# Kernel tuning notes

Measured on AMD Instinct MI355X. Metric: run time of the kernel, lower is better.

## Reference

```python
import jax, jax.numpy as jnp
import numpy as np

EPS = 1e-05

def _self_cost_cosine(embs):
    # embs: [n, d] -> cost: [n, n]
    energy = jnp.sqrt(jnp.sum(embs ** 2, axis=1, keepdims=True))  # [n,1]
    gram = embs @ embs.T
    denom = energy @ energy.T + EPS
    return 1.0 - jnp.exp(-5.0 * (1.0 - gram / denom))

def _mutual_cost_cosine(embs1, embs2):
    e1 = jnp.sqrt(jnp.sum(embs1 ** 2, axis=1, keepdims=True))
    e2 = jnp.sqrt(jnp.sum(embs2 ** 2, axis=1, keepdims=True))
    gram = embs1 @ embs2.T
    denom = e1 @ e2.T + EPS
    return 1.0 - jnp.exp(-(1.0 - gram / denom))

def _tensor_times_mat_l2(cost_s, cost_t, trans, mu_s, mu_t):
    f1 = (cost_s ** 2) @ mu_s            # [n1,1], broadcasts over columns
    f2 = mu_t.T @ (cost_t ** 2).T        # [1,n2], broadcasts over rows
    return f1 + f2 - 2.0 * (cost_s @ trans @ cost_t.T)

def _similarity_l2(cost_pred, cost_truth):
    return jnp.sum((cost_pred - cost_truth) ** 2 * jnp.exp(-cost_truth))

def _orthogonal(embs):
    d = embs.shape[1]
    orth = embs.T @ embs - jnp.eye(d, dtype=embs.dtype)
    return jnp.sum(orth ** 2)

def setup_inputs() -> dict:
    key = jax.random.key(0)
    ks = jax.random.split(key, 9)
    num1, num2, dim, n = 50000, 50000, 128, 4096
    emb1_w = jax.random.uniform(ks[0], (num1, dim), jnp.float32, -1.0 / dim, 1.0 / dim)
    emb2_w = jax.random.uniform(ks[1], (num2, dim), jnp.float32, -1.0 / dim, 1.0 / dim)
    index1 = jax.random.randint(ks[2], (n,), 0, num1, dtype=jnp.int64 if jax.config.jax_enable_x64 else jnp.int32)
    index2 = jax.random.randint(ks[3], (n,), 0, num2, dtype=jnp.int64 if jax.config.jax_enable_x64 else jnp.int32)
    trans = jax.random.uniform(ks[4], (n, n), jnp.float32) / (n * n)
    mu_s = jax.random.uniform(ks[5], (n, 1), jnp.float32) / n
    mu_t = jax.random.uniform(ks[6], (n, 1), jnp.float32) / n
    cost1 = jax.random.uniform(ks[7], (n, n), jnp.float32)
    cost2 = jax.random.uniform(ks[8], (n, n), jnp.float32)
    return {"index1": index1, "index2": index2, "trans": trans, "mu_s": mu_s,
            "mu_t": mu_t, "cost1": cost1, "cost2": cost2,
            "emb1_w": emb1_w, "emb2_w": emb2_w}

def reference(index1, index2, trans, mu_s, mu_t, cost1, cost2, emb1_w, emb2_w):
    embs1 = emb1_w[index1]  # [n1, d]
    embs2 = emb2_w[index2]  # [n2, d]
    cost_s = _self_cost_cosine(embs1)
    cost_t = _self_cost_cosine(embs2)
    cost_st = _mutual_cost_cosine(embs1, embs2)
    cost = _tensor_times_mat_l2(cost_s, cost_t, trans, mu_s, mu_t)
    d_gw = jnp.sum(cost * trans)
    d_w = jnp.sum(cost_st * trans)
    regularizer = (_similarity_l2(cost_s, cost1) + _similarity_l2(cost_t, cost2)
                   + _orthogonal(embs1) + _orthogonal(embs2))
    return (d_gw, d_w, regularizer)
```

## Files before the change

kernel.cpp:

```cpp
#include <hip/hip_runtime.h>
#include <math.h>

#define N 4096
#define D 128
#define FEPS 1e-5f
#define C0F 0.993262053f
#define NT 64

typedef __attribute__((ext_vector_type(8))) short bf16x8;
typedef __attribute__((ext_vector_type(4))) float f32x4;

__device__ __forceinline__ unsigned short f2bf(float f) {
    union { float f; unsigned u; } v; v.f = f;
    unsigned r = v.u + 0x7fffu + ((v.u >> 16) & 1u);
    return (unsigned short)(r >> 16);
}
__device__ __forceinline__ float bf2f(short s) {
    union { unsigned u; float f; } v; v.u = ((unsigned)(unsigned short)s) << 16;
    return v.f;
}

__device__ __forceinline__ void async16(void* lds, const void* g) {
    __builtin_amdgcn_global_load_lds(
        (const __attribute__((address_space(1))) unsigned int*)g,
        (__attribute__((address_space(3))) unsigned int*)lds, 16, 0, 0);
}

__device__ __forceinline__ double block_reduce256(double v, double* red) {
    int t = threadIdx.x;
    red[t] = v;
    __syncthreads();
    #pragma unroll
    for (int s = 128; s > 0; s >>= 1) {
        if (t < s) red[t] += red[t + s];
        __syncthreads();
    }
    double r = red[0];
    __syncthreads();
    return r;
}

__device__ __forceinline__ double block_reduce512(double v, double* red) {
    int t = threadIdx.x;
    red[t] = v;
    __syncthreads();
    #pragma unroll
    for (int s = 256; s > 0; s >>= 1) {
        if (t < s) red[t] += red[t + s];
        __syncthreads();
    }
    double r = red[0];
    __syncthreads();
    return r;
}

__global__ void gather_energy(const float* __restrict__ W, const int* __restrict__ idx,
                              float* __restrict__ E, float* __restrict__ energy) {
    int i = blockIdx.x, t = threadIdx.x;
    float v = W[(size_t)idx[i] * D + t];
    E[(size_t)i * D + t] = v;
    float sq = v * v;
    #pragma unroll
    for (int o = 32; o > 0; o >>= 1) sq += __shfl_down(sq, o);
    __shared__ float s2[2];
    if ((t & 63) == 0) s2[t >> 6] = sq;
    __syncthreads();
    if (t == 0) energy[i] = sqrtf(s2[0] + s2[1]);
}

__global__ void trans_convert(const float* __restrict__ T,
                              unsigned short* __restrict__ Ta,
                              unsigned short* __restrict__ Tb,
                              float* __restrict__ trow, float* __restrict__ tcol,
                              double* __restrict__ sc) {
    __shared__ float cs[4][256];
    __shared__ float ws[4];
    int t = threadIdx.x;
    int cb = blockIdx.x * 64 + (t & 63);
    int rb = blockIdx.y * 4 + (t >> 6);
    int r0 = rb * 4, c0 = cb * 4;
    float vv[4][4];
    #pragma unroll
    for (int i = 0; i < 4; ++i) {
        float4 r4 = *(const float4*)&T[(size_t)(r0 + i) * N + c0];
        vv[i][0] = r4.x; vv[i][1] = r4.y; vv[i][2] = r4.z; vv[i][3] = r4.w;
    }
    #pragma unroll
    for (int i = 0; i < 4; ++i) {
        int r = r0 + i;
        size_t slot = ((size_t)(r >> 4) * (N / 8) + (c0 >> 3)) * 128 + (r & 15) * 8 + (c0 & 7);
        short4 s;
        s.x = (short)f2bf(vv[i][0]); s.y = (short)f2bf(vv[i][1]);
        s.z = (short)f2bf(vv[i][2]); s.w = (short)f2bf(vv[i][3]);
        *(short4*)&Ta[slot] = s;
    }
    #pragma unroll
    for (int j = 0; j < 4; ++j) {
        int n = c0 + j;
        size_t slot = ((size_t)(n >> 4) * (N / 8) + (r0 >> 3)) * 128 + (n & 15) * 8 + (r0 & 7);
        short4 s;
        s.x = (short)f2bf(vv[0][j]); s.y = (short)f2bf(vv[1][j]);
        s.z = (short)f2bf(vv[2][j]); s.w = (short)f2bf(vv[3][j]);
        *(short4*)&Tb[slot] = s;
    }
    float wtot = 0.f;
    #pragma unroll
    for (int i = 0; i < 4; ++i) {
        float s = vv[i][0] + vv[i][1] + vv[i][2] + vv[i][3];
        #pragma unroll
        for (int o = 32; o > 0; o >>= 1) s += __shfl_down(s, o);
        if ((t & 63) == 0) { atomicAdd(&trow[r0 + i], s); wtot += s; }
    }
    if ((t & 63) == 0) ws[t >> 6] = wtot;
    int g = t >> 6;
    #pragma unroll
    for (int j = 0; j < 4; ++j)
        cs[g][(t & 63) * 4 + j] = vv[0][j] + vv[1][j] + vv[2][j] + vv[3][j];
    __syncthreads();
    float csum = cs[0][t] + cs[1][t] + cs[2][t] + cs[3][t];
    atomicAdd(&tcol[blockIdx.x * 256 + t], csum);
    if (t == 0) atomicAdd(&sc[5], (double)(ws[0] + ws[1] + ws[2] + ws[3]));
}

template <int SELF>
__global__ __launch_bounds__(256) void cost_kernel(
        const float* __restrict__ EA, const float* __restrict__ EB,
        const float* __restrict__ ea, const float* __restrict__ eb,
        const float* __restrict__ ref_or_trans,
        const float* __restrict__ mu, const float* __restrict__ tsum,
        unsigned short* __restrict__ outD, double* __restrict__ sc) {
    __shared__ float As[16][68];
    __shared__ float Bs[16][68];
    __shared__ double red[256];
    int t = threadIdx.x;
    int tx = t & 15, ty = t >> 4;
    int bi = blockIdx.y * 64, bj = blockIdx.x * 64;
    float acc[4][4] = {};
    for (int kk = 0; kk < D; kk += 16) {
        #pragma unroll
        for (int r = 0; r < 4; ++r) {
            int e = t + 256 * r;
            int ar = e >> 4, ac = e & 15;
            As[ac][ar] = EA[(size_t)(bi + ar) * D + kk + ac];
            Bs[ac][ar] = EB[(size_t)(bj + ar) * D + kk + ac];
        }
        __syncthreads();
        #pragma unroll
        for (int k = 0; k < 16; ++k) {
            float4 av = *(const float4*)&As[k][ty * 4];
            float4 bv = *(const float4*)&Bs[k][tx * 4];
            float a[4] = {av.x, av.y, av.z, av.w};
            float b[4] = {bv.x, bv.y, bv.z, bv.w};
            #pragma unroll
            for (int u = 0; u < 4; ++u)
                #pragma unroll
                for (int v = 0; v < 4; ++v)
                    acc[u][v] = fmaf(a[u], b[v], acc[u][v]);
        }
        __syncthreads();
    }
    float eav[4], ebv[4];
    #pragma unroll
    for (int u = 0; u < 4; ++u) eav[u] = ea[bi + ty * 4 + u];
    #pragma unroll
    for (int v = 0; v < 4; ++v) ebv[v] = eb[bj + tx * 4 + v];

    double l1 = 0.0, l2 = 0.0;
    #pragma unroll
    for (int u = 0; u < 4; ++u) {
        int ri = bi + ty * 4 + u;
        float cv[4];
        #pragma unroll
        for (int v = 0; v < 4; ++v) {
            int ci = bj + tx * 4 + v;
            size_t id = (size_t)ri * N + ci;
            float denom = eav[u] * ebv[v] + FEPS;
            float cosv = acc[u][v] / denom;
            if (SELF) {
                float c = 1.f - expf(-5.f * (1.f - cosv));
                cv[v] = c;
                float rc = ref_or_trans[id];
                float dd = c - rc;
                l1 += (double)(dd * dd * expf(-rc));
                l2 += (double)(c * c) * (double)mu[ci] * (double)tsum[ri];
            } else {
                float c = 1.f - expf(-(1.f - cosv));
                l1 += (double)c * (double)ref_or_trans[id];
            }
        }
        if (SELF) {
            int ci0 = bj + tx * 4;
            size_t slot = ((size_t)(ri >> 4) * (N / 8) + (ci0 >> 3)) * 128 + (ri & 15) * 8 + (ci0 & 7);
            short4 s;
            s.x = (short)f2bf(cv[0] - C0F); s.y = (short)f2bf(cv[1] - C0F);
            s.z = (short)f2bf(cv[2] - C0F); s.w = (short)f2bf(cv[3] - C0F);
            *(short4*)&outD[slot] = s;
        }
    }
    double s1 = block_reduce256(l1, red);
    if (SELF) {
        double s2v = block_reduce256(l2, red);
        if (t == 0) { atomicAdd(&sc[0], s1); atomicAdd(&sc[1], s2v); }
    } else {
        if (t == 0) atomicAdd(&sc[3], s1);
    }
}

#define MFMA16(a, b, c) __builtin_amdgcn_mfma_f32_16x16x32_bf16(a, b, c, 0, 0, 0)

template <int STORE>
__global__ __launch_bounds__(512, 2) void gemm_mfma(
        const unsigned short* __restrict__ Ag, const unsigned short* __restrict__ Bg,
        unsigned short* __restrict__ Pdb,
        const float* __restrict__ trow, const float* __restrict__ tcol,
        double* __restrict__ sc) {
    __shared__ __align__(16) char Lds[131072];
    __shared__ double red[512];
    const int t = threadIdx.x, l = t & 63;
    const int w = __builtin_amdgcn_readfirstlane(t >> 6);
    const int wm = w >> 2, wn = w & 3;
    const int lid = blockIdx.x;
    const int swz = (lid & 7) * 32 + (lid >> 3);
    const int by = swz >> 4, bx = swz & 15;
    const size_t GRP = (size_t)(N / 8) * 256;

    const char* aBase = (const char*)Ag + ((size_t)by * 16 + w) * GRP + (size_t)l * 16;
    const char* bBase = (const char*)Bg + ((size_t)bx * 16 + w) * GRP + (size_t)l * 16;

#define ISSUE_A(KH, TT) do {                                                   \
    char* _d = Lds + ((TT) & 1) * 65536 + (KH) * 16384 + w * 1024;             \
    const char* _g = aBase + (size_t)(TT) * 2048 + (KH) * 1024;                \
    async16(_d, _g); async16(_d + 8192, _g + 8 * GRP); } while (0)
#define ISSUE_B(KH, TT) do {                                                   \
    char* _d = Lds + ((TT) & 1) * 65536 + 32768 + (KH) * 16384 + w * 1024;     \
    const char* _g = bBase + (size_t)(TT) * 2048 + (KH) * 1024;                \
    async16(_d, _g); async16(_d + 8192, _g + 8 * GRP); } while (0)

    f32x4 acc[8][4];
    #pragma unroll
    for (int i = 0; i < 8; ++i)
        #pragma unroll
        for (int j = 0; j < 4; ++j)
            acc[i][j] = (f32x4){0.f, 0.f, 0.f, 0.f};

    ISSUE_A(0, 0); ISSUE_B(0, 0); ISSUE_A(1, 0); ISSUE_B(1, 0); ISSUE_A(0, 1);
    asm volatile("s_waitcnt vmcnt(6)" ::: "memory");
    __builtin_amdgcn_s_barrier();
    asm volatile("" ::: "memory");

    bf16x8 af[8];
    const char* Albase = Lds + wm * 8192;
    const char* Blbase = Lds + 32768 + wn * 4096;

    for (int tt = 0; tt < NT; ++tt) {
        const int bufo = (tt & 1) * 65536;
        {
            const char* Ab = Albase + bufo;
            const char* Bb = Blbase + bufo;
            #pragma unroll
            for (int mf = 0; mf < 8; ++mf)
                af[mf] = *(const bf16x8*)(Ab + mf * 1024 + l * 16);
            bf16x8 b0 = *(const bf16x8*)(Bb + l * 16);
            bf16x8 b1 = *(const bf16x8*)(Bb + 1024 + l * 16);
            if (tt + 1 < NT) ISSUE_B(0, tt + 1);
            __builtin_amdgcn_s_setprio(1);
            #pragma unroll
            for (int mf = 0; mf < 8; ++mf) {
                acc[mf][0] = MFMA16(af[mf], b0, acc[mf][0]);
                acc[mf][1] = MFMA16(af[mf], b1, acc[mf][1]);
            }
            __builtin_amdgcn_s_setprio(0);
            asm volatile("" ::: "memory");
            __builtin_amdgcn_s_barrier();
            asm volatile("" ::: "memory");
        }
        {
            const char* Bb = Blbase + bufo + 2048;
            bf16x8 b0 = *(const bf16x8*)(Bb + l * 16);
            bf16x8 b1 = *(const bf16x8*)(Bb + 1024 + l * 16);
            if (tt + 1 < NT) ISSUE_A(1, tt + 1);
            __builtin_amdgcn_s_setprio(1);
            #pragma unroll
            for (int mf = 0; mf < 8; ++mf) {
                acc[mf][2] = MFMA16(af[mf], b0, acc[mf][2]);
                acc[mf][3] = MFMA16(af[mf], b1, acc[mf][3]);
            }
            __builtin_amdgcn_s_setprio(0);
            if (tt < NT - 1) { asm volatile("s_waitcnt vmcnt(6)" ::: "memory"); }
            else             { asm volatile("s_waitcnt vmcnt(0)" ::: "memory"); }
            asm volatile("" ::: "memory");
            __builtin_amdgcn_s_barrier();
            asm volatile("" ::: "memory");
        }
        {
            const char* Ab = Albase + bufo + 16384;
            const char* Bb = Blbase + bufo + 16384;
            #pragma unroll
            for (int mf = 0; mf < 8; ++mf)
                af[mf] = *(const bf16x8*)(Ab + mf * 1024 + l * 16);
            bf16x8 b0 = *(const bf16x8*)(Bb + l * 16);
            bf16x8 b1 = *(const bf16x8*)(Bb + 1024 + l * 16);
            if (tt + 1 < NT) ISSUE_B(1, tt + 1);
            __builtin_amdgcn_s_setprio(1);
            #pragma unroll
            for (int mf = 0; mf < 8; ++mf) {
                acc[mf][0] = MFMA16(af[mf], b0, acc[mf][0]);
                acc[mf][1] = MFMA16(af[mf], b1, acc[mf][1]);
            }
            __builtin_amdgcn_s_setprio(0);
            asm volatile("" ::: "memory");
            __builtin_amdgcn_s_barrier();
            asm volatile("" ::: "memory");
        }
        {
            const char* Bb = Blbase + bufo + 16384 + 2048;
            bf16x8 b0 = *(const bf16x8*)(Bb + l * 16);
            bf16x8 b1 = *(const bf16x8*)(Bb + 1024 + l * 16);
            if (tt + 2 < NT) ISSUE_A(0, tt + 2);
            __builtin_amdgcn_s_setprio(1);
            #pragma unroll
            for (int mf = 0; mf < 8; ++mf) {
                acc[mf][2] = MFMA16(af[mf], b0, acc[mf][2]);
                acc[mf][3] = MFMA16(af[mf], b1, acc[mf][3]);
            }
            __builtin_amdgcn_s_setprio(0);
            if (tt < NT - 2)       { asm volatile("s_waitcnt vmcnt(6)" ::: "memory"); }
            else if (tt == NT - 2) { asm volatile("s_waitcnt vmcnt(4)" ::: "memory"); }
            asm volatile("" ::: "memory");
            __builtin_amdgcn_s_barrier();
            asm volatile("" ::: "memory");
        }
    }
#undef ISSUE_A
#undef ISSUE_B

    const size_t base = ((size_t)(by * 16 + bx)) * 65536 + (size_t)w * 8192;
    if (STORE) {
        #pragma unroll
        for (int mf = 0; mf < 8; ++mf)
            #pragma unroll
            for (int nf = 0; nf < 4; ++nf) {
                f32x4 a = acc[mf][nf];
                short4 s;
                s.x = (short)f2bf(a[0]); s.y = (short)f2bf(a[1]);
                s.z = (short)f2bf(a[2]); s.w = (short)f2bf(a[3]);
                *(short4*)&Pdb[base + (size_t)(mf * 4 + nf) * 256 + (size_t)l * 4] = s;
            }
    } else {
        double t1 = 0.0, t2 = 0.0, t3 = 0.0;
        const int quad = l >> 4, lan = l & 15;
        #pragma unroll
        for (int mf = 0; mf < 8; ++mf) {
            const int ib = by * 256 + wm * 128 + mf * 16 + quad * 4;
            float4 tr4 = *(const float4*)&trow[ib];
            float trv[4] = {tr4.x, tr4.y, tr4.z, tr4.w};
            #pragma unroll
            for (int nf = 0; nf < 4; ++nf) {
                const int j = bx * 256 + wn * 64 + nf * 16 + lan;
                const float tcj = tcol[j];
                short4 p = *(const short4*)&Pdb[base + (size_t)(mf * 4 + nf) * 256 + (size_t)l * 4];
                float pf[4] = {bf2f(p.x), bf2f(p.y), bf2f(p.z), bf2f(p.w)};
                #pragma unroll
                for (int r = 0; r < 4; ++r) {
                    double x = (double)acc[mf][nf][r];
                    t1 += (double)tcj * x;
                    t2 += (double)trv[r] * (double)pf[r];
                    t3 += x * (double)pf[r];
                }
            }
        }
        double s1 = block_reduce512(t1, red);
        double s2 = block_reduce512(t2, red);
        double s3 = block_reduce512(t3, red);
        if (t == 0) {
            atomicAdd(&sc[6], s1);
            atomicAdd(&sc[7], s2);
            atomicAdd(&sc[2], s3);
        }
    }
}

__global__ __launch_bounds__(256) void gram_partial(const float* __restrict__ E,
                                                    float* __restrict__ G) {
    __shared__ float Es[16][132];
    int t = threadIdx.x, tx = t & 15, ty = t >> 4;
    int i0 = blockIdx.x * 128;
    float acc[8][8] = {};
    for (int kk = 0; kk < 128; kk += 16) {
        #pragma unroll
        for (int r = 0; r < 2; ++r) {
            int q = t + 256 * r;
            int row = q >> 5, c4 = (q & 31) * 4;
            *(float4*)&Es[row][c4] = *(const float4*)&E[(size_t)(i0 + kk + row) * D + c4];
        }
        __syncthreads();
        #pragma unroll
        for (int k = 0; k < 16; ++k) {
            float a[8], b[8];
            *(float4*)&a[0] = *(const float4*)&Es[k][ty * 8];
            *(float4*)&a[4] = *(const float4*)&Es[k][ty * 8 + 4];
            *(float4*)&b[0] = *(const float4*)&Es[k][tx * 8];
            *(float4*)&b[4] = *(const float4*)&Es[k][tx * 8 + 4];
            #pragma unroll
            for (int u = 0; u < 8; ++u)
                #pragma unroll
                for (int v = 0; v < 8; ++v)
                    acc[u][v] = fmaf(a[u], b[v], acc[u][v]);
        }
        __syncthreads();
    }
    #pragma unroll
    for (int u = 0; u < 8; ++u)
        #pragma unroll
        for (int v = 0; v < 8; ++v)
            atomicAdd(&G[(size_t)(ty * 8 + u) * D + tx * 8 + v], acc[u][v]);
}

__global__ void orth_final(const float* __restrict__ G, double* __restrict__ sc) {
    __shared__ double red[256];
    const float* g = G + (size_t)blockIdx.x * D * D;
    int t = threadIdx.x;
    double s = 0.0;
    for (int q = t; q < D * D; q += 256) {
        float v = g[q] - ((q % (D + 1)) == 0 ? 1.f : 0.f);
        s += (double)v * (double)v;
    }
    double r = block_reduce256(s, red);
    if (t == 0) atomicAdd(&sc[4], r);
}

__global__ void finalize(const double* __restrict__ sc, float* __restrict__ out) {
    if (threadIdx.x == 0) {
        const double C0 = (double)C0F;
        double S = sc[5];
        double pq = C0 * C0 * S * S + C0 * sc[6] + C0 * sc[7] + sc[2];
        out[0] = (float)(sc[1] - 2.0 * pq);
        out[1] = (float)sc[3];
        out[2] = (float)(sc[0] + sc[4]);
    }
}

extern "C" void kernel_launch(void* const* d_in, const int* in_sizes, int n_in,
                              void* d_out, int out_size, void* d_ws, size_t ws_size,
                              hipStream_t stream) {
    const int*   index1 = (const int*)d_in[0];
    const int*   index2 = (const int*)d_in[1];
    const float* trans  = (const float*)d_in[2];
    const float* mu_s   = (const float*)d_in[3];
    const float* mu_t   = (const float*)d_in[4];
    const float* cost1  = (const float*)d_in[5];
    const float* cost2  = (const float*)d_in[6];
    const float* emb1_w = (const float*)d_in[7];
    const float* emb2_w = (const float*)d_in[8];
    float* out = (float*)d_out;

    char* w = (char*)d_ws;
    double* sc  = (double*)w;
    float* tcol = (float*)(w + 256);
    float* trow = (float*)(w + 16640);
    float* e1   = (float*)(w + 33024);
    float* e2   = (float*)(w + 49408);
    float* E1   = (float*)(w + 65792);
    float* E2   = (float*)(w + 2162944);
    unsigned short* Ds  = (unsigned short*)(w + 4260096);
    unsigned short* Ta  = (unsigned short*)(w + 37814528);
    unsigned short* Tb  = (unsigned short*)(w + 71368960);
    unsigned short* Pdb = (unsigned short*)(w + 104923392);
    float* Gbuf = (float*)(w + 37814528);

    hipMemsetAsync(d_ws, 0, 33024, stream);

    gather_energy<<<N, D, 0, stream>>>(emb1_w, index1, E1, e1);
    gather_energy<<<N, D, 0, stream>>>(emb2_w, index2, E2, e2);
    trans_convert<<<dim3(16, 256), 256, 0, stream>>>(trans, Ta, Tb, trow, tcol, sc);

    dim3 g64(N / 64, N / 64);

    cost_kernel<1><<<g64, 256, 0, stream>>>(E1, E1, e1, e1, cost1, mu_s, trow, Ds, sc);
    gemm_mfma<1><<<256, 512, 0, stream>>>(Ds, Tb, Pdb, nullptr, nullptr, sc);
    cost_kernel<1><<<g64, 256, 0, stream>>>(E2, E2, e2, e2, cost2, mu_t, tcol, Ds, sc);
    gemm_mfma<0><<<256, 512, 0, stream>>>(Ta, Ds, Pdb, trow, tcol, sc);
    cost_kernel<0><<<g64, 256, 0, stream>>>(E1, E2, e1, e2, trans, nullptr, nullptr, nullptr, sc);
    hipMemsetAsync(Gbuf, 0, 2 * D * D * sizeof(float), stream);
    gram_partial<<<32, 256, 0, stream>>>(E1, Gbuf);
    gram_partial<<<32, 256, 0, stream>>>(E2, Gbuf + D * D);
    orth_final<<<2, 256, 0, stream>>>(Gbuf, sc);

    finalize<<<1, 64, 0, stream>>>(sc, out);
}
```

Before: 954.9 us.

## Restructure MFMA main loop into M-quarter phases with deeper async prefetch

The GEMM inner loop now splits each k-half into two phases over half the M fragments, each using all four B fragments, instead of phases over half the N fragments. Each phase does 16 MFMAs on 4 A plus 4 B registers, which lowers live fragment registers. Global-to-LDS prefetch is moved earlier: B for tile tt+2 is issued one iteration ahead, and the vmcnt thresholds are raised to match. Extra barriers per phase and lgkmcnt waits are added, which adds sync cost and makes correctness depend on the new buffer-reuse ordering.

Result: slower. 982.4 us (+2.9%).

```diff
diff --git a/kernel.cpp b/kernel.cpp
--- a/kernel.cpp
+++ b/kernel.cpp
@@ -223,9 +223,10 @@
     const int swz = (lid & 7) * 32 + (lid >> 3);
     const int by = swz >> 4, bx = swz & 15;
     const size_t GRP = (size_t)(N / 8) * 256;
-
-    const char* aBase = (const char*)Ag + ((size_t)by * 16 + w) * GRP + (size_t)l * 16;
-    const char* bBase = (const char*)Bg + ((size_t)bx * 16 + w) * GRP + (size_t)l * 16;
+    const int l16 = l * 16;
+
+    const char* aBase = (const char*)Ag + ((size_t)by * 16 + w) * GRP + (size_t)l16;
+    const char* bBase = (const char*)Bg + ((size_t)bx * 16 + w) * GRP + (size_t)l16;
 
 #define ISSUE_A(KH, TT) do {                                                   \
     char* _d = Lds + ((TT) & 1) * 65536 + (KH) * 16384 + w * 1024;             \
@@ -243,96 +244,86 @@
         for (int j = 0; j < 4; ++j)
             acc[i][j] = (f32x4){0.f, 0.f, 0.f, 0.f};
 
-    ISSUE_A(0, 0); ISSUE_B(0, 0); ISSUE_A(1, 0); ISSUE_B(1, 0); ISSUE_A(0, 1);
-    asm volatile("s_waitcnt vmcnt(6)" ::: "memory");
+    ISSUE_A(0, 0); ISSUE_B(0, 0); ISSUE_A(1, 0); ISSUE_B(1, 0);
+    ISSUE_A(0, 1); ISSUE_B(0, 1);
+    asm volatile("s_waitcnt vmcnt(8)" ::: "memory");
     __builtin_amdgcn_s_barrier();
     asm volatile("" ::: "memory");
 
-    bf16x8 af[8];
     const char* Albase = Lds + wm * 8192;
     const char* Blbase = Lds + 32768 + wn * 4096;
 
+    bf16x8 aq[4], b0, b1, b2, b3;
+
+#define MFMA_Q(MB) do {                                                        \
+    _Pragma("unroll")                                                          \
+    for (int _i = 0; _i < 4; ++_i) {                                           \
+        acc[(MB) + _i][0] = MFMA16(aq[_i], b0, acc[(MB) + _i][0]);             \
+        acc[(MB) + _i][1] = MFMA16(aq[_i], b1, acc[(MB) + _i][1]);             \
+        acc[(MB) + _i][2] = MFMA16(aq[_i], b2, acc[(MB) + _i][2]);             \
+        acc[(MB) + _i][3] = MFMA16(aq[_i], b3, acc[(MB) + _i][3]);             \
+    } } while (0)
+
+#define REGION_END                                                             \
+    asm volatile("s_waitcnt lgkmcnt(0)" ::: "memory");                         \
+    __builtin_amdgcn_s_barrier();                                              \
+    asm volatile("" ::: "memory");
+
     for (int tt = 0; tt < NT; ++tt) {
         const int bufo = (tt & 1) * 65536;
-        {
-            const char* Ab = Albase + bufo;
-            const char* Bb = Blbase + bufo;
-            #pragma unroll
-            for (int mf = 0; mf < 8; ++mf)
-                af[mf] = *(const bf16x8*)(Ab + mf * 1024 + l * 16);
-            bf16x8 b0 = *(const bf16x8*)(Bb + l * 16);
-            bf16x8 b1 = *(const bf16x8*)(Bb + 1024 + l * 16);
-            if (tt + 1 < NT) ISSUE_B(0, tt + 1);
-            __builtin_amdgcn_s_setprio(1);
-            #pragma unroll
-            for (int mf = 0; mf < 8; ++mf) {
-                acc[mf][0] = MFMA16(af[mf], b0, acc[mf][0]);
-                acc[mf][1] = MFMA16(af[mf], b1, acc[mf][1]);
-            }
-            __builtin_amdgcn_s_setprio(0);
-            asm volatile("" ::: "memory");
-            __builtin_amdgcn_s_barrier();
-            asm volatile("" ::: "memory");
-        }
-        {
-            const char* Bb = Blbase + bufo + 2048;
-            bf16x8 b0 = *(const bf16x8*)(Bb + l * 16);
-            bf16x8 b1 = *(const bf16x8*)(Bb + 1024 + l * 16);
-            if (tt + 1 < NT) ISSUE_A(1, tt + 1);
-            __builtin_amdgcn_s_setprio(1);
-            #pragma unroll
-            for (int mf = 0; mf < 8; ++mf) {
-                acc[mf][2] = MFMA16(af[mf], b0, acc[mf][2]);
-                acc[mf][3] = MFMA16(af[mf], b1, acc[mf][3]);
-            }
-            __builtin_amdgcn_s_setprio(0);
-            if (tt < NT - 1) { asm volatile("s_waitcnt vmcnt(6)" ::: "memory"); }
-            else             { asm volatile("s_waitcnt vmcnt(0)" ::: "memory"); }
-            asm volatile("" ::: "memory");
-            __builtin_amdgcn_s_barrier();
-            asm volatile("" ::: "memory");
-        }
-        {
-            const char* Ab = Albase + bufo + 16384;
-            const char* Bb = Blbase + bufo + 16384;
-            #pragma unroll
-            for (int mf = 0; mf < 8; ++mf)
-                af[mf] = *(const bf16x8*)(Ab + mf * 1024 + l * 16);
-            bf16x8 b0 = *(const bf16x8*)(Bb + l * 16);
-            bf16x8 b1 = *(const bf16x8*)(Bb + 1024 + l * 16);
-            if (tt + 1 < NT) ISSUE_B(1, tt + 1);
-            __builtin_amdgcn_s_setprio(1);
-            #pragma unroll
-            for (int mf = 0; mf < 8; ++mf) {
-                acc[mf][0] = MFMA16(af[mf], b0, acc[mf][0]);
-                acc[mf][1] = MFMA16(af[mf], b1, acc[mf][1]);
-            }
-            __builtin_amdgcn_s_setprio(0);
-            asm volatile("" ::: "memory");
-            __builtin_amdgcn_s_barrier();
-            asm volatile("" ::: "memory");
-        }
-        {
-            const char* Bb = Blbase + bufo + 16384 + 2048;
-            bf16x8 b0 = *(const bf16x8*)(Bb + l * 16);
-            bf16x8 b1 = *(const bf16x8*)(Bb + 1024 + l * 16);
-            if (tt + 2 < NT) ISSUE_A(0, tt + 2);
-            __builtin_amdgcn_s_setprio(1);
-            #pragma unroll
-            for (int mf = 0; mf < 8; ++mf) {
-                acc[mf][2] = MFMA16(af[mf], b0, acc[mf][2]);
-                acc[mf][3] = MFMA16(af[mf], b1, acc[mf][3]);
-            }
-            __builtin_amdgcn_s_setprio(0);
-            if (tt < NT - 2)       { asm volatile("s_waitcnt vmcnt(6)" ::: "memory"); }
-            else if (tt == NT - 2) { asm volatile("s_waitcnt vmcnt(4)" ::: "memory"); }
-            asm volatile("" ::: "memory");
-            __builtin_amdgcn_s_barrier();
-            asm volatile("" ::: "memory");
-        }
+        const char* Ab0 = Albase + bufo;
+        const char* Bb0 = Blbase + bufo;
+        const char* Ab1 = Ab0 + 16384;
+        const char* Bb1 = Bb0 + 16384;
+        #pragma unroll
+        for (int i = 0; i < 4; ++i) aq[i] = *(const bf16x8*)(Ab0 + i * 1024 + l16);
+        b0 = *(const bf16x8*)(Bb0 + l16);
+        b1 = *(const bf16x8*)(Bb0 + 1024 + l16);
+        b2 = *(const bf16x8*)(Bb0 + 2048 + l16);
+        b3 = *(const bf16x8*)(Bb0 + 3072 + l16);
+        if (tt + 1 < NT) { ISSUE_A(1, tt + 1); ISSUE_B(1, tt + 1); }
+        __builtin_amdgcn_s_barrier();
+        __builtin_amdgcn_s_setprio(1);
+        MFMA_Q(0);
+        __builtin_amdgcn_s_setprio(0);
+        REGION_END
+        #pragma unroll
+        for (int i = 0; i < 4; ++i) aq[i] = *(const bf16x8*)(Ab0 + (4 + i) * 1024 + l16);
+        if (tt + 2 < NT) ISSUE_B(0, tt + 2);
+        __builtin_amdgcn_s_barrier();
+        __builtin_amdgcn_s_setprio(1);
+        MFMA_Q(4);
+        __builtin_amdgcn_s_setprio(0);
+        if (tt < NT - 2)       { asm volatile("s_waitcnt vmcnt(10)" ::: "memory"); }
+        else if (tt == NT - 2) { asm volatile("s_waitcnt vmcnt(8)" ::: "memory"); }
+        else                   { asm volatile("s_waitcnt vmcnt(0)" ::: "memory"); }
+        REGION_END
+        #pragma unroll
+        for (int i = 0; i < 4; ++i) aq[i] = *(const bf16x8*)(Ab1 + i * 1024 + l16);
+        b0 = *(const bf16x8*)(Bb1 + l16);
+        b1 = *(const bf16x8*)(Bb1 + 1024 + l16);
+        b2 = *(const bf16x8*)(Bb1 + 2048 + l16);
+        b3 = *(const bf16x8*)(Bb1 + 3072 + l16);
+        if (tt + 2 < NT) ISSUE_A(0, tt + 2);
+        __builtin_amdgcn_s_barrier();
+        __builtin_amdgcn_s_setprio(1);
+        MFMA_Q(0);
+        __builtin_amdgcn_s_setprio(0);
+        REGION_END
+        #pragma unroll
+        for (int i = 0; i < 4; ++i) aq[i] = *(const bf16x8*)(Ab1 + (4 + i) * 1024 + l16);
+        __builtin_amdgcn_s_barrier();
+        __builtin_amdgcn_s_setprio(1);
+        MFMA_Q(4);
+        __builtin_amdgcn_s_setprio(0);
+        if (tt < NT - 2)       { asm volatile("s_waitcnt vmcnt(8)" ::: "memory"); }
+        else if (tt == NT - 2) { asm volatile("s_waitcnt vmcnt(4)" ::: "memory"); }
+        REGION_END
     }
 #undef ISSUE_A
 #undef ISSUE_B
+#undef MFMA_Q
+#undef REGION_END
 
     const size_t base = ((size_t)(by * 16 + bx)) * 65536 + (size_t)w * 8192;
     if (STORE) {
```
